# Kernel optimization log

Hardware: AMD Instinct MI355X
Metric: run time of the kernel (lower is better)

## Reference

```python
import jax, jax.numpy as jnp
import numpy as np

# db4 decomposition low-pass filter, pywt coefficient order
DEC_LO = np.array([-0.010597401784997278, 0.032883011666982945,
                   0.030841381835986965, -0.18703481171888114,
                   -0.02798376941698385, 0.6308807679295904,
                   0.7148465705525415, 0.23037781330885523], dtype=np.float32)
LEVEL = 5
B, C, L = 64, 64, 8192


def _qmf_hi(dec_lo):
    # pywt relation: dec_hi[n] = (-1)^(n+1) * dec_lo[F-1-n]
    F = dec_lo.shape[0]
    signs = jnp.where(jnp.arange(F) % 2 == 0, -1.0, 1.0).astype(dec_lo.dtype)
    return signs * dec_lo[::-1]


def _wavedec(x, dec_lo, dec_hi):
    # pywt.dwt(v, w, 'symmetric') == np.convolve(sym_pad(v, F-1), filt, 'valid')[1::2]
    # implemented as a stride-2 cross-correlation with the reversed filter.
    b, c, n = x.shape
    v = x.reshape(b * c, n)
    F = dec_lo.shape[0]
    # kernel: (out_ch=2 [lo, hi], in_ch=1, width=F); reversed => true convolution
    k = jnp.stack([dec_lo[::-1], dec_hi[::-1]])[:, None, :]
    details = []
    for _ in range(LEVEL):
        ext = jnp.pad(v, ((0, 0), (F - 1, F - 1)), mode='symmetric')[:, 1:]
        y = jax.lax.conv_general_dilated(ext[:, None, :], k,
                                         window_strides=(2,), padding='VALID')
        v = y[:, 0, :]           # approximation -> next level input
        details.append(y[:, 1, :])  # detail for this level (finest first)
    approx = v.reshape(b, c, -1)
    # pywt order: [cA_L, cD_L, ..., cD_1] -> coarsest detail first
    det = [d.reshape(b, c, -1) for d in reversed(details)]
    return (approx, *det)


def setup_inputs() -> dict:
    key = jax.random.key(0)
    x = jax.random.normal(key, (B, C, L), dtype=jnp.float32)
    dec_lo = jnp.asarray(DEC_LO)
    dec_hi = _qmf_hi(dec_lo)
    return {"x": x, "dec_lo": dec_lo, "dec_hi": dec_hi}


def reference(x, dec_lo, dec_hi):
    # Returns (cA_L, cD_L, cD_{L-1}, ..., cD_1), matching the torch module's
    # [approx_tensor, detail_tensors] flattened.
    return _wavedec(x, dec_lo, dec_hi)
```

## Files before the change

### kernel.cpp

```cpp
#include <hip/hip_runtime.h>


static constexpr int ROWS = 4096;
static constexpr int N0 = 8192;
static constexpr int L1n = 4099, L2n = 2053, L3n = 1030, L4n = 518, L5n = 262;
static constexpr size_t OFF_D5 = 1073152u;
static constexpr size_t OFF_D4 = 2146304u;
static constexpr size_t OFF_D3 = 4268032u;
static constexpr size_t OFF_D2 = 8486912u;
static constexpr size_t OFF_D1 = 16896000u;

__device__ __forceinline__ void barrier_lds() {
    asm volatile("s_waitcnt lgkmcnt(0)\n\ts_barrier" ::: "memory");
}

__device__ __forceinline__ float refl_load(const float* __restrict__ s, int idx, int n) {
    int i = (idx < 0) ? (-1 - idx) : ((idx >= n) ? (2 * n - 1 - idx) : idx);
    return s[i];
}

template <int N>
__device__ __forceinline__ void load_window(const float* __restrict__ src,
                                            int j, float* __restrict__ w) {
    constexpr int jmax = (N - 10) >> 3;
    const int jb = j < 1 ? 1 : (j > jmax ? jmax : j);
    const float2* __restrict__ s2 = reinterpret_cast<const float2*>(src) + (4 * jb - 3);
#pragma unroll
    for (int t = 0; t < 8; ++t) {
        const float2 v = s2[t];
        w[2 * t] = v.x; w[2 * t + 1] = v.y;
    }
}

template <int N, int M>
__device__ __forceinline__ void edge_group(
    const float* __restrict__ src,
    const float* __restrict__ h, const float* __restrict__ g,
    float* __restrict__ adst, float* __restrict__ ddst, int j)
{
#pragma unroll 4
    for (int r = 0; r < 4; ++r) {
        const int pos = 4 * j + r;
        if (pos >= M) break;
        const int s0 = 2 * pos + 1;
        float a = 0.f, d = 0.f;
#pragma unroll
        for (int q = 0; q < 8; ++q) {
            const float v = refl_load(src, s0 - q, N);
            a = fmaf(h[q], v, a);
            d = fmaf(g[q], v, d);
        }
        ddst[pos] = d;
        adst[pos] = a;
    }
}

template <int N, int M, int NITER>
__device__ __forceinline__ void dwt_level(
    const float* __restrict__ src,
    const float* __restrict__ h, const float* __restrict__ g,
    float* __restrict__ adst, float* __restrict__ ddst, int tid)
{
    constexpr int ngroups = (M + 3) >> 2;
    constexpr int jmax = (N - 10) >> 3;
    constexpr int rem = ngroups - NITER * 256;
    constexpr bool full = (NITER * 256 <= ngroups);

    float w[NITER][16];
#pragma unroll
    for (int t = 0; t < NITER; ++t) {
        const int j = tid + t * 256;
        if (full || j < ngroups)
            load_window<N>(src, j, &w[t][0]);
    }
    __builtin_amdgcn_sched_barrier(0);

#pragma unroll
    for (int t = 0; t < NITER; ++t) {
        const int j = tid + t * 256;
        if (!full && j >= ngroups) break;
        const int p0 = 4 * j;
        if (j >= 1 && j <= jmax && p0 + 3 < M) {
            float aa[4], dd[4];
#pragma unroll
            for (int r = 0; r < 4; ++r) {
                float a = 0.f, d = 0.f;
#pragma unroll
                for (int q = 0; q < 8; ++q) {
                    const float v = w[t][2 * r + 7 - q];
                    a = fmaf(h[q], v, a);
                    d = fmaf(g[q], v, d);
                }
                aa[r] = a; dd[r] = d;
            }
#pragma unroll
            for (int r = 0; r < 4; ++r) ddst[p0 + r] = dd[r];
#pragma unroll
            for (int r = 0; r < 4; ++r) adst[p0 + r] = aa[r];
        } else {
            edge_group<N, M>(src, h, g, adst, ddst, j);
        }
    }
    if constexpr (rem > 0) {
        if (tid < rem)
            edge_group<N, M>(src, h, g, adst, ddst, NITER * 256 + tid);
    }
}

__global__ __launch_bounds__(256, 4)
void wavedec5_kernel(const float* __restrict__ x,
                     const float* __restrict__ dlo,
                     const float* __restrict__ dhi,
                     float* __restrict__ out)
{
    __shared__ __align__(16) float bufA[4100];
    __shared__ __align__(16) float bufB[2056];

    const int row = blockIdx.x;
    const int tid = threadIdx.x;

    float h[8], g[8];
#pragma unroll
    for (int i = 0; i < 8; ++i) { h[i] = dlo[i]; g[i] = dhi[i]; }

    const float* __restrict__ xr = x + (size_t)row * N0;

    dwt_level<N0, L1n, 4>(xr, h, g, bufA,
                          out + OFF_D1 + (size_t)row * L1n, tid);
    barrier_lds();
    dwt_level<L1n, L2n, 2>(bufA, h, g, bufB,
                           out + OFF_D2 + (size_t)row * L2n, tid);
    barrier_lds();
    dwt_level<L2n, L3n, 1>(bufB, h, g, bufA,
                           out + OFF_D3 + (size_t)row * L3n, tid);
    barrier_lds();
    dwt_level<L3n, L4n, 1>(bufA, h, g, bufB,
                           out + OFF_D4 + (size_t)row * L4n, tid);
    barrier_lds();
    dwt_level<L4n, L5n, 1>(bufB, h, g,
                           out + (size_t)row * L5n,
                           out + OFF_D5 + (size_t)row * L5n, tid);
}

extern "C" void kernel_launch(void* const* d_in, const int* in_sizes, int n_in,
                              void* d_out, int out_size, void* d_ws, size_t ws_size,
                              hipStream_t stream) {
    const float* x   = (const float*)d_in[0];
    const float* dlo = (const float*)d_in[1];
    const float* dhi = (const float*)d_in[2];
    float* out = (float*)d_out;
    wavedec5_kernel<<<ROWS, 256, 0, stream>>>(x, dlo, dhi, out);
}
```

Before: 58.68 us.

## Spill level-2 approximation to global workspace to cut LDS and raise occupancy

```diff
diff --git a/kernel.cpp b/kernel.cpp
--- a/kernel.cpp
+++ b/kernel.cpp
@@ -9,6 +9,9 @@
 static constexpr size_t OFF_D3 = 4268032u;
 static constexpr size_t OFF_D2 = 8486912u;
 static constexpr size_t OFF_D1 = 16896000u;
+
+static constexpr int WS_STRIDE = 2056;
+static constexpr size_t WS_NEED = (size_t)ROWS * WS_STRIDE * sizeof(float);
 
 __device__ __forceinline__ void barrier_lds() {
     asm volatile("s_waitcnt lgkmcnt(0)\n\ts_barrier" ::: "memory");
@@ -107,11 +110,49 @@
     }
 }
 
+__global__ __launch_bounds__(256, 8)
+void wavedec5_hiocc(const float* __restrict__ x,
+                    const float* __restrict__ dlo,
+                    const float* __restrict__ dhi,
+                    float* __restrict__ out,
+                    float* __restrict__ ws)
+{
+    __shared__ __align__(16) float bufA[4100];
+
+    const int row = blockIdx.x;
+    const int tid = threadIdx.x;
+
+    float h[8], g[8];
+#pragma unroll
+    for (int i = 0; i < 8; ++i) { h[i] = dlo[i]; g[i] = dhi[i]; }
+
+    const float* __restrict__ xr = x + (size_t)row * N0;
+    float* __restrict__ a2g = ws + (size_t)row * WS_STRIDE;
+    float* __restrict__ a3p = bufA;
+    float* __restrict__ a4p = bufA + 2048;
+
+    dwt_level<N0, L1n, 4>(xr, h, g, bufA,
+                          out + OFF_D1 + (size_t)row * L1n, tid);
+    barrier_lds();
+    dwt_level<L1n, L2n, 2>(bufA, h, g, a2g,
+                           out + OFF_D2 + (size_t)row * L2n, tid);
+    __syncthreads();
+    dwt_level<L2n, L3n, 1>(a2g, h, g, a3p,
+                           out + OFF_D3 + (size_t)row * L3n, tid);
+    barrier_lds();
+    dwt_level<L3n, L4n, 1>(a3p, h, g, a4p,
+                           out + OFF_D4 + (size_t)row * L4n, tid);
+    barrier_lds();
+    dwt_level<L4n, L5n, 1>(a4p, h, g,
+                           out + (size_t)row * L5n,
+                           out + OFF_D5 + (size_t)row * L5n, tid);
+}
+
 __global__ __launch_bounds__(256, 4)
-void wavedec5_kernel(const float* __restrict__ x,
-                     const float* __restrict__ dlo,
-                     const float* __restrict__ dhi,
-                     float* __restrict__ out)
+void wavedec5_lds(const float* __restrict__ x,
+                  const float* __restrict__ dlo,
+                  const float* __restrict__ dhi,
+                  float* __restrict__ out)
 {
     __shared__ __align__(16) float bufA[4100];
     __shared__ __align__(16) float bufB[2056];
@@ -149,5 +190,9 @@
     const float* dlo = (const float*)d_in[1];
     const float* dhi = (const float*)d_in[2];
     float* out = (float*)d_out;
-    wavedec5_kernel<<<ROWS, 256, 0, stream>>>(x, dlo, dhi, out);
+    if (ws_size >= WS_NEED && d_ws != nullptr) {
+        wavedec5_hiocc<<<ROWS, 256, 0, stream>>>(x, dlo, dhi, out, (float*)d_ws);
+    } else {
+        wavedec5_lds<<<ROWS, 256, 0, stream>>>(x, dlo, dhi, out);
+    }
 }
```

New measurement: 106.8 us. 1.82x slower.
